# Performance work log

Hardware: AMD Instinct MI355X
Metric: run time of the kernel (lower is better)

The kernel has to match this reference:

```python
import jax, jax.numpy as jnp
import numpy as np

N = 100000      # nodes
E = 2500000     # edges
DIN, H, DOUT = 3, 32, 4
EPS = 1e-5

def _lin(k, i, o):
    kw, kb = jax.random.split(k)
    lim = 1.0 / np.sqrt(i)
    W = jax.random.uniform(kw, (i, o), jnp.float32, -lim, lim)
    b = jax.random.uniform(kb, (o,), jnp.float32, -lim, lim)
    return W, b

def setup_inputs():
    key = jax.random.key(0)
    ks = jax.random.split(key, 12)
    x = jax.random.normal(ks[0], (N, DIN), jnp.float32)
    edge_index = jax.random.randint(ks[1], (2, E), 0, N, dtype=jnp.int32)
    w_in1, b_in1 = _lin(ks[2], DIN, H)
    w_in2, b_in2 = _lin(ks[3], H, H)
    gamma = jnp.ones((H,), jnp.float32)
    beta = jnp.zeros((H,), jnp.float32)
    wg1, bg1 = _lin(ks[4], H, H)
    wg2, bg2 = _lin(ks[5], H, H)
    wg3, bg3 = _lin(ks[6], H, H)
    wo1, bo1 = _lin(ks[7], H, H)
    wo2, bo2 = _lin(ks[8], H, H)
    wo3, bo3 = _lin(ks[9], H, DOUT)
    return dict(x=x, w_in1=w_in1, b_in1=b_in1, w_in2=w_in2, b_in2=b_in2,
                gamma=gamma, beta=beta,
                wg1=wg1, bg1=bg1, wg2=wg2, bg2=bg2, wg3=wg3, bg3=bg3,
                wo1=wo1, bo1=bo1, wo2=wo2, bo2=bo2, wo3=wo3, bo3=bo3,
                edge_index=edge_index)

def _gcn(h, W, b, src, dst, norm):
    # PyG GCNConv: x' = scatter_add(norm * (xW)[src] -> dst) + bias
    hw = h @ W                                   # [N, H]
    msg = hw[src] * norm[:, None]                # [E+N, H] gather + scale
    out = jax.ops.segment_sum(msg, dst, num_segments=N)
    return out + b

def reference(x, w_in1, b_in1, w_in2, b_in2, gamma, beta,
              wg1, bg1, wg2, bg2, wg3, bg3,
              wo1, bo1, wo2, bo2, wo3, bo3, edge_index):
    leaky = lambda v: jax.nn.leaky_relu(v, 0.01)
    # input MLP
    h = leaky(x @ w_in1 + b_in1)
    h = leaky(h @ w_in2 + b_in2)
    # BatchNorm1d (training-mode batch statistics, biased variance)
    mu = jnp.mean(h, axis=0)
    var = jnp.mean((h - mu) ** 2, axis=0)
    h = (h - mu) * jax.lax.rsqrt(var + EPS) * gamma + beta
    # gcn_norm with self-loops: deg over target index, sym normalization
    loop = jnp.arange(N, dtype=edge_index.dtype)
    src = jnp.concatenate([edge_index[0], loop])
    dst = jnp.concatenate([edge_index[1], loop])
    deg = jax.ops.segment_sum(jnp.ones_like(src, jnp.float32), dst, num_segments=N)
    dis = jax.lax.rsqrt(deg)                     # deg >= 1 due to self-loops
    norm = dis[src] * dis[dst]                   # [E+N]
    h = jax.nn.elu(_gcn(h, wg1, bg1, src, dst, norm))
    h = jax.nn.elu(_gcn(h, wg2, bg2, src, dst, norm))
    h = jax.nn.elu(_gcn(h, wg3, bg3, src, dst, norm))
    # output MLP
    r = leaky(h @ wo1 + bo1)
    r = leaky(r @ wo2 + bo2)
    r = r @ wo3 + bo3                            # [N, 4]
    r = r.at[:, 0].set(jax.nn.sigmoid(r[:, 0]))
    return r
```

## Files before the change

### kernel.cpp

```cpp
#include <hip/hip_runtime.h>
#include <hip/hip_fp16.h>

#define HF 32
#define EPS 1e-5f
#define BSH 7
#define BSZ 128
#define CH  8192
#define SUBCAP 512
#define CAP (8*SUBCAP)

typedef int vi4 __attribute__((ext_vector_type(4)));

__device__ __forceinline__ float leaky(float v){ return fmaxf(v, 0.01f*v); }
__device__ __forceinline__ float elu1(float v){ return v > 0.f ? v : (expf(v)-1.f); }
__device__ __forceinline__ float sigmoidf(float v){ return 1.f/(1.f+expf(-v)); }

__device__ __forceinline__ int4 nt_load_i4(const int* p){
    vi4 v = __builtin_nontemporal_load((const vi4*)p);
    return make_int4(v.x, v.y, v.z, v.w);
}

__device__ __forceinline__ void addrow8(float* a, float4 v){
    const __half2* p = (const __half2*)&v;
#pragma unroll
    for (int k = 0; k < 4; k++){
        float2 f = __half22float2(p[k]);
        a[2*k] += f.x; a[2*k+1] += f.y;
    }
}
__device__ __forceinline__ float4 h2add4f(float4 a, float4 b){
    __half2* pa = (__half2*)&a; __half2* pb = (__half2*)&b;
    float4 r; __half2* pr = (__half2*)&r;
#pragma unroll
    for (int k = 0; k < 4; k++) pr[k] = __hadd2(pa[k], pb[k]);
    return r;
}

union SMem {
    struct {
        float sW1[3*HF]; float sB1[HF]; float sW2[HF*HF]; float sB2[HF];
        float sh[256][33];
    } mlp;
    struct { int lcnt[1024]; int lbase[1024]; int lpos[1024]; } bin;
};

__global__ __launch_bounds__(256)
void k_mlp_bin(const float* __restrict__ x,
               const float* __restrict__ w1, const float* __restrict__ b1,
               const float* __restrict__ w2, const float* __restrict__ b2,
               __half* __restrict__ h, float* __restrict__ stats,
               const int* __restrict__ src, const int* __restrict__ dst,
               int* __restrict__ gfill, int* __restrict__ ep,
               int N, int E, int B, int NB1){
    __shared__ SMem sm;
    int t = threadIdx.x;
    if ((int)blockIdx.x < NB1){
        for (int i = t; i < 3*HF; i += 256) sm.mlp.sW1[i] = w1[i];
        if (t < HF){ sm.mlp.sB1[t] = b1[t]; sm.mlp.sB2[t] = b2[t]; }
        for (int i = t; i < HF*HF; i += 256) sm.mlp.sW2[i] = w2[i];
        __syncthreads();
        int n = blockIdx.x*256 + t;
        float h2[HF];
        if (n < N){
            float x0 = x[(size_t)n*3], x1 = x[(size_t)n*3+1], x2 = x[(size_t)n*3+2];
            float h1[HF];
#pragma unroll
            for (int j = 0; j < HF; j++){
                float v = fmaf(x0, sm.mlp.sW1[j], fmaf(x1, sm.mlp.sW1[HF+j],
                          fmaf(x2, sm.mlp.sW1[2*HF+j], sm.mlp.sB1[j])));
                h1[j] = leaky(v);
            }
#pragma unroll
            for (int j = 0; j < HF; j++){
                float v = sm.mlp.sB2[j];
#pragma unroll
                for (int i = 0; i < HF; i++) v = fmaf(h1[i], sm.mlp.sW2[i*HF+j], v);
                h2[j] = leaky(v);
            }
            float4* hv = (float4*)(h + (size_t)n*HF);
#pragma unroll
            for (int jb = 0; jb < 4; jb++){
                __half2 hh[4];
#pragma unroll
                for (int k = 0; k < 4; k++)
                    hh[k] = __float22half2_rn(make_float2(h2[jb*8+2*k], h2[jb*8+2*k+1]));
                hv[jb] = *(float4*)hh;
            }
        } else {
#pragma unroll
            for (int j = 0; j < HF; j++) h2[j] = 0.f;
        }
#pragma unroll
        for (int j = 0; j < HF; j++) sm.mlp.sh[t][j] = h2[j];
        __syncthreads();
        int f = t & 31, g = t >> 5;
        float s = 0.f, ss = 0.f;
        for (int i = 0; i < 32; i++){
            float v = sm.mlp.sh[g*32 + i][f];
            s += v; ss += v*v;
        }
        __syncthreads();
        sm.mlp.sh[g][f] = s; sm.mlp.sh[8+g][f] = ss;
        __syncthreads();
        if (t < HF){
            float a = 0.f, b = 0.f;
#pragma unroll
            for (int g2 = 0; g2 < 8; g2++){ a += sm.mlp.sh[g2][t]; b += sm.mlp.sh[8+g2][t]; }
            atomicAdd(&stats[t], a);
            atomicAdd(&stats[HF+t], b);
        }
    } else {
        int bid = blockIdx.x - NB1;
        for (int i = t; i < B; i += 256){ sm.bin.lcnt[i] = 0; sm.bin.lpos[i] = 0; }
        __syncthreads();
        int base = bid * CH;
        int xcd = blockIdx.x & 7;
        int dv[16], sv[16];
        for (int half = 0; half < 2; half++){
            int hbase = base + half*4096;
#pragma unroll
            for (int i = 0; i < 16; i++){
                int e = hbase + t + i*256;
                dv[i] = (e < E) ? dst[e] : -1;
                sv[i] = (e < E) ? src[e] : 0;
            }
#pragma unroll
            for (int i = 0; i < 16; i++)
                if (dv[i] >= 0) atomicAdd(&sm.bin.lcnt[dv[i] >> BSH], 1);
            if (half == 0){
            }
            __syncthreads();
            if (half == 0){
            }
        }
        for (int i = t; i < B; i += 256){
            int c = sm.bin.lcnt[i];
            sm.bin.lbase[i] = c ? (i*CAP + xcd*SUBCAP + atomicAdd(&gfill[i*8 + xcd], c)) : 0;
        }
        __syncthreads();
        for (int half = 0; half < 2; half++){
            int hbase = base + half*4096;
#pragma unroll
            for (int i = 0; i < 16; i++){
                int e = hbase + t + i*256;
                if (e < E){
                    int d = dst[e], s = src[e];
                    int bb = d >> BSH;
                    int p = sm.bin.lbase[bb] + atomicAdd(&sm.bin.lpos[bb], 1);
                    ep[p] = (s << BSH) | (d & (BSZ-1));
                }
            }
        }
    }
}

__global__ __launch_bounds__(256)
void k_bucketD(int* __restrict__ ep, const int* __restrict__ gfill,
               int2* __restrict__ rowp2, float* __restrict__ dis, int N, int B){
    __shared__ int sep[CAP];
    __shared__ int lcnt[256], lpre[256], lfill[256], sc[256];
    int b = blockIdx.x, t = threadIdx.x;
    int cx[8], coff[8], cnt = 0;
#pragma unroll
    for (int x = 0; x < 8; x++){ cx[x] = gfill[b*8 + x]; coff[x] = cnt; cnt += cx[x]; }
    lcnt[t] = 0; lfill[t] = 0;
    __syncthreads();
    int base = b*CAP;
#pragma unroll
    for (int x = 0; x < 8; x++)
        for (int j = t; j < cx[x]; j += 256) sep[coff[x] + j] = ep[base + x*SUBCAP + j];
    __syncthreads();
    for (int e = t; e < cnt; e += 256) atomicAdd(&lcnt[sep[e] & (BSZ-1)], 1);
    __syncthreads();
    int v = lcnt[t];
    sc[t] = v; __syncthreads();
    for (int off = 1; off < 256; off <<= 1){
        int u = (t >= off) ? sc[t - off] : 0;
        __syncthreads();
        sc[t] += u;
        __syncthreads();
    }
    int pre = sc[t] - v;
    lpre[t] = pre;
    int n = b*BSZ + t;
    if (t < BSZ && n < N){
        rowp2[n] = make_int2(base + pre, base + pre + v);
        dis[n]   = rsqrtf((float)(v + 1));
    }
    __syncthreads();
    for (int e = t; e < cnt; e += 256){
        int val = sep[e];
        int d = val & (BSZ-1);
        int p = lpre[d] + atomicAdd(&lfill[d], 1);
        ep[base + p] = val >> BSH;
    }
}

__global__ __launch_bounds__(256)
void k_bn_t1(const __half* __restrict__ h, const float* __restrict__ stats,
             const float* __restrict__ gamma, const float* __restrict__ beta,
             const float* __restrict__ W, const float* __restrict__ dis,
             __half* __restrict__ tout, int N){
    __shared__ float sW[HF*HF];
    __shared__ float sh[64][33];
    int tid = threadIdx.x;
    for (int i = tid; i < HF*HF; i += 256) sW[i] = W[i];
    int nib = tid >> 2, l = tid & 3;
    int n = blockIdx.x*64 + nib;
    float hv[8];
    float d = 0.f;
    if (n < N){
        float4 raw = ((const float4*)h)[(size_t)n*4 + l];
        const __half2* p = (const __half2*)&raw;
        float tmp[8];
#pragma unroll
        for (int k = 0; k < 4; k++){
            float2 f2 = __half22float2(p[k]);
            tmp[2*k] = f2.x; tmp[2*k+1] = f2.y;
        }
        d = dis[n];
        float inv = 1.0f / (float)N;
#pragma unroll
        for (int c = 0; c < 8; c++){
            int f = 8*l + c;
            float mu  = stats[f]    * inv;
            float var = stats[HF+f] * inv - mu*mu;
            float rs  = rsqrtf(var + EPS);
            hv[c] = (tmp[c] - mu) * rs * gamma[f] + beta[f];
        }
    } else {
#pragma unroll
        for (int c = 0; c < 8; c++) hv[c] = 0.f;
    }
    __syncthreads();
#pragma unroll
    for (int c = 0; c < 8; c++) sh[nib][8*l + c] = hv[c];
    __syncthreads();
    float o[8] = {0.f,0.f,0.f,0.f,0.f,0.f,0.f,0.f};
#pragma unroll
    for (int i = 0; i < HF; i++){
        float hvv = sh[nib][i];
        float4 w0 = *(const float4*)&sW[i*HF + 8*l];
        float4 w1 = *(const float4*)&sW[i*HF + 8*l + 4];
        o[0] = fmaf(hvv, w0.x, o[0]); o[1] = fmaf(hvv, w0.y, o[1]);
        o[2] = fmaf(hvv, w0.z, o[2]); o[3] = fmaf(hvv, w0.w, o[3]);
        o[4] = fmaf(hvv, w1.x, o[4]); o[5] = fmaf(hvv, w1.y, o[5]);
        o[6] = fmaf(hvv, w1.z, o[6]); o[7] = fmaf(hvv, w1.w, o[7]);
    }
    if (n < N){
        __half2 hh[4];
#pragma unroll
        for (int k = 0; k < 4; k++)
            hh[k] = __float22half2_rn(make_float2(o[2*k]*d, o[2*k+1]*d));
        ((float4*)tout)[(size_t)n*4 + l] = *(float4*)hh;
    }
}

__global__ __launch_bounds__(256)
void k_gather_t(const __half* __restrict__ tin, const int* __restrict__ esrc,
                const int2* __restrict__ rowp2, const float* __restrict__ dis,
                const float* __restrict__ bias, const float* __restrict__ W,
                __half* __restrict__ tout, int N){
    __shared__ float sW[HF*HF];
    __shared__ float sh[64][33];
    int tid = threadIdx.x;
    for (int i = tid; i < HF*HF; i += 256) sW[i] = W[i];
    int nib = tid >> 2, l = tid & 3;
    int n = blockIdx.x*64 + nib;
    float acc[8] = {0.f,0.f,0.f,0.f,0.f,0.f,0.f,0.f};
    float d = 0.f;
    const float4* tv = (const float4*)tin;
    if (n < N){
        addrow8(acc, tv[(size_t)n*4 + l]);
        int2 r = rowp2[n];
        int e = r.x, e1 = r.y;
        while (e < e1 && (e & 3)){ addrow8(acc, tv[(size_t)esrc[e]*4 + l]); e++; }
        for (; e + 7 < e1; e += 8){
            int4 a4 = nt_load_i4(&esrc[e]);
            int4 b4 = nt_load_i4(&esrc[e+4]);
            float4 v0 = tv[(size_t)a4.x*4 + l];
            float4 v1 = tv[(size_t)a4.y*4 + l];
            float4 v2 = tv[(size_t)a4.z*4 + l];
            float4 v3 = tv[(size_t)a4.w*4 + l];
            float4 v4 = tv[(size_t)b4.x*4 + l];
            float4 v5 = tv[(size_t)b4.y*4 + l];
            float4 v6 = tv[(size_t)b4.z*4 + l];
            float4 v7 = tv[(size_t)b4.w*4 + l];
            addrow8(acc, h2add4f(h2add4f(v0, v1), h2add4f(v2, v3)));
            addrow8(acc, h2add4f(h2add4f(v4, v5), h2add4f(v6, v7)));
        }
        for (; e + 3 < e1; e += 4){
            int4 s4 = nt_load_i4(&esrc[e]);
            float4 v0 = tv[(size_t)s4.x*4 + l];
            float4 v1 = tv[(size_t)s4.y*4 + l];
            float4 v2 = tv[(size_t)s4.z*4 + l];
            float4 v3 = tv[(size_t)s4.w*4 + l];
            addrow8(acc, h2add4f(h2add4f(v0, v1), h2add4f(v2, v3)));
        }
        for (; e < e1; e++) addrow8(acc, tv[(size_t)esrc[e]*4 + l]);
        d = dis[n];
#pragma unroll
        for (int c = 0; c < 8; c++)
            acc[c] = elu1(fmaf(d, acc[c], bias[8*l + c]));
    }
    __syncthreads();
#pragma unroll
    for (int c = 0; c < 8; c++) sh[nib][8*l + c] = acc[c];
    __syncthreads();
    float o[8] = {0.f,0.f,0.f,0.f,0.f,0.f,0.f,0.f};
#pragma unroll
    for (int i = 0; i < HF; i++){
        float hvv = sh[nib][i];
        float4 w0 = *(const float4*)&sW[i*HF + 8*l];
        float4 w1 = *(const float4*)&sW[i*HF + 8*l + 4];
        o[0] = fmaf(hvv, w0.x, o[0]); o[1] = fmaf(hvv, w0.y, o[1]);
        o[2] = fmaf(hvv, w0.z, o[2]); o[3] = fmaf(hvv, w0.w, o[3]);
        o[4] = fmaf(hvv, w1.x, o[4]); o[5] = fmaf(hvv, w1.y, o[5]);
        o[6] = fmaf(hvv, w1.z, o[6]); o[7] = fmaf(hvv, w1.w, o[7]);
    }
    if (n < N){
        __half2 hh[4];
#pragma unroll
        for (int k = 0; k < 4; k++)
            hh[k] = __float22half2_rn(make_float2(o[2*k]*d, o[2*k+1]*d));
        ((float4*)tout)[(size_t)n*4 + l] = *(float4*)hh;
    }
}

__global__ __launch_bounds__(256)
void k_gather_out(const __half* __restrict__ tin, const int* __restrict__ esrc,
                  const int2* __restrict__ rowp2, const float* __restrict__ dis,
                  const float* __restrict__ bg3,
                  const float* __restrict__ wo1, const float* __restrict__ bo1,
                  const float* __restrict__ wo2, const float* __restrict__ bo2,
                  const float* __restrict__ wo3, const float* __restrict__ bo3,
                  float* __restrict__ out, int N){
    __shared__ float sW1[HF*HF], sW2[HF*HF], sW3[HF*4];
    __shared__ float sh[64][33], sh2[64][33];
    int tid = threadIdx.x;
    for (int i = tid; i < HF*HF; i += 256){ sW1[i] = wo1[i]; sW2[i] = wo2[i]; }
    if (tid < HF*4) sW3[tid] = wo3[tid];
    int nib = tid >> 2, l = tid & 3;
    int n = blockIdx.x*64 + nib;
    float acc[8] = {0.f,0.f,0.f,0.f,0.f,0.f,0.f,0.f};
    const float4* tv = (const float4*)tin;
    if (n < N){
        addrow8(acc, tv[(size_t)n*4 + l]);
        int2 r = rowp2[n];
        int e = r.x, e1 = r.y;
        while (e < e1 && (e & 3)){ addrow8(acc, tv[(size_t)esrc[e]*4 + l]); e++; }
        for (; e + 7 < e1; e += 8){
            int4 a4 = nt_load_i4(&esrc[e]);
            int4 b4 = nt_load_i4(&esrc[e+4]);
            float4 v0 = tv[(size_t)a4.x*4 + l];
            float4 v1 = tv[(size_t)a4.y*4 + l];
            float4 v2 = tv[(size_t)a4.z*4 + l];
            float4 v3 = tv[(size_t)a4.w*4 + l];
            float4 v4 = tv[(size_t)b4.x*4 + l];
            float4 v5 = tv[(size_t)b4.y*4 + l];
            float4 v6 = tv[(size_t)b4.z*4 + l];
            float4 v7 = tv[(size_t)b4.w*4 + l];
            addrow8(acc, h2add4f(h2add4f(v0, v1), h2add4f(v2, v3)));
            addrow8(acc, h2add4f(h2add4f(v4, v5), h2add4f(v6, v7)));
        }
        for (; e + 3 < e1; e += 4){
            int4 s4 = nt_load_i4(&esrc[e]);
            float4 v0 = tv[(size_t)s4.x*4 + l];
            float4 v1 = tv[(size_t)s4.y*4 + l];
            float4 v2 = tv[(size_t)s4.z*4 + l];
            float4 v3 = tv[(size_t)s4.w*4 + l];
            addrow8(acc, h2add4f(h2add4f(v0, v1), h2add4f(v2, v3)));
        }
        for (; e < e1; e++) addrow8(acc, tv[(size_t)esrc[e]*4 + l]);
        float d = dis[n];
#pragma unroll
        for (int c = 0; c < 8; c++)
            acc[c] = elu1(fmaf(d, acc[c], bg3[8*l + c]));
    }
    __syncthreads();
#pragma unroll
    for (int c = 0; c < 8; c++) sh[nib][8*l + c] = acc[c];
    __syncthreads();
    float o1[8];
#pragma unroll
    for (int c = 0; c < 8; c++) o1[c] = bo1[8*l + c];
#pragma unroll
    for (int i = 0; i < HF; i++){
        float hvv = sh[nib][i];
        float4 w0 = *(const float4*)&sW1[i*HF + 8*l];
        float4 w1 = *(const float4*)&sW1[i*HF + 8*l + 4];
        o1[0] = fmaf(hvv, w0.x, o1[0]); o1[1] = fmaf(hvv, w0.y, o1[1]);
        o1[2] = fmaf(hvv, w0.z, o1[2]); o1[3] = fmaf(hvv, w0.w, o1[3]);
        o1[4] = fmaf(hvv, w1.x, o1[4]); o1[5] = fmaf(hvv, w1.y, o1[5]);
        o1[6] = fmaf(hvv, w1.z, o1[6]); o1[7] = fmaf(hvv, w1.w, o1[7]);
    }
#pragma unroll
    for (int c = 0; c < 8; c++) sh2[nib][8*l + c] = leaky(o1[c]);
    __syncthreads();
    float o2[8];
#pragma unroll
    for (int c = 0; c < 8; c++) o2[c] = bo2[8*l + c];
#pragma unroll
    for (int i = 0; i < HF; i++){
        float hvv = sh2[nib][i];
        float4 w0 = *(const float4*)&sW2[i*HF + 8*l];
        float4 w1 = *(const float4*)&sW2[i*HF + 8*l + 4];
        o2[0] = fmaf(hvv, w0.x, o2[0]); o2[1] = fmaf(hvv, w0.y, o2[1]);
        o2[2] = fmaf(hvv, w0.z, o2[2]); o2[3] = fmaf(hvv, w0.w, o2[3]);
        o2[4] = fmaf(hvv, w1.x, o2[4]); o2[5] = fmaf(hvv, w1.y, o2[5]);
        o2[6] = fmaf(hvv, w1.z, o2[6]); o2[7] = fmaf(hvv, w1.w, o2[7]);
    }
#pragma unroll
    for (int c = 0; c < 8; c++) sh[nib][8*l + c] = leaky(o2[c]);
    __syncthreads();
    if (n < N){
        float v = bo3[l];
#pragma unroll
        for (int i = 0; i < HF; i++) v = fmaf(sh[nib][i], sW3[i*4 + l], v);
        if (l == 0) v = sigmoidf(v);
        out[(size_t)n*4 + l] = v;
    }
}

extern "C" void kernel_launch(void* const* d_in, const int* in_sizes, int n_in,
                              void* d_out, int out_size, void* d_ws, size_t ws_size,
                              hipStream_t stream) {
    const float* x     = (const float*)d_in[0];
    const float* w_in1 = (const float*)d_in[1];
    const float* b_in1 = (const float*)d_in[2];
    const float* w_in2 = (const float*)d_in[3];
    const float* b_in2 = (const float*)d_in[4];
    const float* gamma = (const float*)d_in[5];
    const float* beta  = (const float*)d_in[6];
    const float* wg1   = (const float*)d_in[7];
    const float* bg1   = (const float*)d_in[8];
    const float* wg2   = (const float*)d_in[9];
    const float* bg2   = (const float*)d_in[10];
    const float* wg3   = (const float*)d_in[11];
    const float* bg3   = (const float*)d_in[12];
    const float* wo1   = (const float*)d_in[13];
    const float* bo1   = (const float*)d_in[14];
    const float* wo2   = (const float*)d_in[15];
    const float* bo2   = (const float*)d_in[16];
    const float* wo3   = (const float*)d_in[17];
    const float* bo3   = (const float*)d_in[18];
    const int*   ei    = (const int*)d_in[19];

    int N = in_sizes[0] / 3;
    int E = in_sizes[19] / 2;
    int B = (N + BSZ - 1) >> BSH;

    char* w = (char*)d_ws;
    size_t o = 0;
    auto alloc = [&](size_t bytes){ size_t r = o; o = (o + bytes + 255) & ~(size_t)255; return r; };
    float* stats = (float*)(w + alloc(2*HF*sizeof(float)));
    int*   gfill = (int*)  (w + alloc((size_t)B*8*4));
    size_t zero_bytes = o;
    int2*  rowp2 = (int2*) (w + alloc((size_t)N*8));
    float* dis   = (float*)(w + alloc((size_t)N*4));
    int*   ep    = (int*)  (w + alloc((size_t)B*CAP*4));
    __half* bufH = (__half*)(w + alloc((size_t)N*HF*2));
    __half* tA   = (__half*)(w + alloc((size_t)N*HF*2));
    __half* tB   = (__half*)(w + alloc((size_t)N*HF*2));

    hipMemsetAsync(d_ws, 0, zero_bytes, stream);

    const int* src = ei;
    const int* dst = ei + E;
    int NB1 = (N + 255) / 256;
    int NC  = (E + CH - 1) / CH;
    int GB  = (N + 63) / 64;

    k_mlp_bin<<<NB1 + NC, 256, 0, stream>>>(x, w_in1, b_in1, w_in2, b_in2, bufH, stats,
                                            src, dst, gfill, ep, N, E, B, NB1);
    k_bucketD<<<B, 256, 0, stream>>>(ep, gfill, rowp2, dis, N, B);

    k_bn_t1   <<<GB, 256, 0, stream>>>(bufH, stats, gamma, beta, wg1, dis, tA, N);
    k_gather_t<<<GB, 256, 0, stream>>>(tA, ep, rowp2, dis, bg1, wg2, tB, N);
    k_gather_t<<<GB, 256, 0, stream>>>(tB, ep, rowp2, dis, bg2, wg3, tA, N);
    k_gather_out<<<GB, 256, 0, stream>>>(tA, ep, rowp2, dis, bg3,
                                         wo1, bo1, wo2, bo2, wo3, bo3, (float*)d_out, N);
}
```

Baseline: 288.7 us.

## Compute degrees during binning, fuse CSR build with BN transform, degree-sorted gather order

The binning pass now counts node degrees with global atomics, so the bucket kernel no longer needs a shared-memory histogram and scan. It is fused with the BatchNorm plus first-transform kernel into one launch that computes dis directly from deg. Each bucket also ranks its nodes by degree and writes a node order array, which the gather kernels use so that nodes of similar degree share a wavefront and divergence drops. The chunk size is halved and edges are loaded once into registers with vectorized nontemporal loads. In exchange there are global atomics per edge on deg and one extra indirection in the gather kernels.

```diff
diff --git a/kernel.cpp b/kernel.cpp
--- a/kernel.cpp
+++ b/kernel.cpp
@@ -5,7 +5,7 @@
 #define EPS 1e-5f
 #define BSH 7
 #define BSZ 128
-#define CH  8192
+#define CH  4096
 #define SUBCAP 512
 #define CAP (8*SUBCAP)
 
@@ -51,15 +51,58 @@
                __half* __restrict__ h, float* __restrict__ stats,
                const int* __restrict__ src, const int* __restrict__ dst,
                int* __restrict__ gfill, int* __restrict__ ep,
-               int N, int E, int B, int NB1){
+               int* __restrict__ deg,
+               int N, int E, int B, int NC){
     __shared__ SMem sm;
     int t = threadIdx.x;
-    if ((int)blockIdx.x < NB1){
+    if ((int)blockIdx.x < NC){
+        int bid = blockIdx.x;
+        for (int i = t; i < B; i += 256){ sm.bin.lcnt[i] = 0; sm.bin.lpos[i] = 0; }
+        __syncthreads();
+        int base = bid * CH;
+        int xcd = bid & 7;
+        int dv[16], sv[16];
+        if (base + CH <= E){
+#pragma unroll
+            for (int i = 0; i < 4; i++){
+                int4 d4 = nt_load_i4(dst + base + (t + i*256)*4);
+                int4 s4 = nt_load_i4(src + base + (t + i*256)*4);
+                dv[4*i]   = d4.x; dv[4*i+1] = d4.y; dv[4*i+2] = d4.z; dv[4*i+3] = d4.w;
+                sv[4*i]   = s4.x; sv[4*i+1] = s4.y; sv[4*i+2] = s4.z; sv[4*i+3] = s4.w;
+            }
+        } else {
+#pragma unroll
+            for (int i = 0; i < 16; i++){
+                int e = base + t + i*256;
+                dv[i] = (e < E) ? dst[e] : -1;
+                sv[i] = (e < E) ? src[e] : 0;
+            }
+        }
+#pragma unroll
+        for (int i = 0; i < 16; i++)
+            if (dv[i] >= 0){
+                atomicAdd(&sm.bin.lcnt[dv[i] >> BSH], 1);
+                atomicAdd(&deg[dv[i]], 1);
+            }
+        __syncthreads();
+        for (int i = t; i < B; i += 256){
+            int c = sm.bin.lcnt[i];
+            sm.bin.lbase[i] = c ? (i*CAP + xcd*SUBCAP + atomicAdd(&gfill[i*8 + xcd], c)) : 0;
+        }
+        __syncthreads();
+#pragma unroll
+        for (int i = 0; i < 16; i++)
+            if (dv[i] >= 0){
+                int bb = dv[i] >> BSH;
+                int p = sm.bin.lbase[bb] + atomicAdd(&sm.bin.lpos[bb], 1);
+                ep[p] = (sv[i] << BSH) | (dv[i] & (BSZ-1));
+            }
+    } else {
         for (int i = t; i < 3*HF; i += 256) sm.mlp.sW1[i] = w1[i];
         if (t < HF){ sm.mlp.sB1[t] = b1[t]; sm.mlp.sB2[t] = b2[t]; }
         for (int i = t; i < HF*HF; i += 256) sm.mlp.sW2[i] = w2[i];
         __syncthreads();
-        int n = blockIdx.x*256 + t;
+        int n = (blockIdx.x - NC)*256 + t;
         float h2[HF];
         if (n < N){
             float x0 = x[(size_t)n*3], x1 = x[(size_t)n*3+1], x2 = x[(size_t)n*3+2];
@@ -109,156 +152,123 @@
             atomicAdd(&stats[t], a);
             atomicAdd(&stats[HF+t], b);
         }
+    }
+}
+
+union SMem2 {
+    struct { int sep[CAP]; int sdeg[128]; int spre[128]; int sfill[128]; } c;
+    struct { float sW[HF*HF]; float sh[64][33]; } m;
+};
+
+__global__ __launch_bounds__(256)
+void k_csr_bn(int* __restrict__ ep, const int* __restrict__ gfill,
+              const int* __restrict__ deg,
+              int2* __restrict__ rowp2, float* __restrict__ dis,
+              int* __restrict__ norder,
+              const __half* __restrict__ h, const float* __restrict__ stats,
+              const float* __restrict__ gamma, const float* __restrict__ beta,
+              const float* __restrict__ W, __half* __restrict__ tout,
+              int N, int B){
+    __shared__ SMem2 sm;
+    int t = threadIdx.x;
+    if ((int)blockIdx.x < B){
+        int b = blockIdx.x;
+        int cx[8], coff[8], cnt = 0;
+#pragma unroll
+        for (int xx = 0; xx < 8; xx++){ cx[xx] = gfill[b*8 + xx]; coff[xx] = cnt; cnt += cx[xx]; }
+        int base = b*CAP;
+#pragma unroll
+        for (int xx = 0; xx < 8; xx++)
+            for (int j = t; j < cx[xx]; j += 256) sm.c.sep[coff[xx] + j] = ep[base + xx*SUBCAP + j];
+        if (t < 128){
+            sm.c.sfill[t] = 0;
+            int n = b*BSZ + t;
+            sm.c.sdeg[t] = (n < N) ? deg[n] : 0;
+        }
+        __syncthreads();
+        if (t < 128){
+            int dg = sm.c.sdeg[t];
+            int pre = 0, rank = 0;
+            for (int j = 0; j < 128; j++){
+                int dj = sm.c.sdeg[j];
+                if (j < t) pre += dj;
+                if (dj > dg || (dj == dg && j < t)) rank++;
+            }
+            sm.c.spre[t] = pre;
+            int n = b*BSZ + t;
+            if (n < N){
+                rowp2[n] = make_int2(base + pre, base + pre + dg);
+                dis[n]   = rsqrtf((float)dg + 1.0f);
+                norder[b*BSZ + rank] = n;
+            } else {
+                norder[b*BSZ + rank] = -1;
+            }
+        }
+        __syncthreads();
+        for (int e = t; e < cnt; e += 256){
+            int val = sm.c.sep[e];
+            int d = val & (BSZ-1);
+            int p = sm.c.spre[d] + atomicAdd(&sm.c.sfill[d], 1);
+            ep[base + p] = val >> BSH;
+        }
     } else {
-        int bid = blockIdx.x - NB1;
-        for (int i = t; i < B; i += 256){ sm.bin.lcnt[i] = 0; sm.bin.lpos[i] = 0; }
-        __syncthreads();
-        int base = bid * CH;
-        int xcd = blockIdx.x & 7;
-        int dv[16], sv[16];
-        for (int half = 0; half < 2; half++){
-            int hbase = base + half*4096;
-#pragma unroll
-            for (int i = 0; i < 16; i++){
-                int e = hbase + t + i*256;
-                dv[i] = (e < E) ? dst[e] : -1;
-                sv[i] = (e < E) ? src[e] : 0;
-            }
-#pragma unroll
-            for (int i = 0; i < 16; i++)
-                if (dv[i] >= 0) atomicAdd(&sm.bin.lcnt[dv[i] >> BSH], 1);
-            if (half == 0){
-            }
-            __syncthreads();
-            if (half == 0){
-            }
-        }
-        for (int i = t; i < B; i += 256){
-            int c = sm.bin.lcnt[i];
-            sm.bin.lbase[i] = c ? (i*CAP + xcd*SUBCAP + atomicAdd(&gfill[i*8 + xcd], c)) : 0;
-        }
-        __syncthreads();
-        for (int half = 0; half < 2; half++){
-            int hbase = base + half*4096;
-#pragma unroll
-            for (int i = 0; i < 16; i++){
-                int e = hbase + t + i*256;
-                if (e < E){
-                    int d = dst[e], s = src[e];
-                    int bb = d >> BSH;
-                    int p = sm.bin.lbase[bb] + atomicAdd(&sm.bin.lpos[bb], 1);
-                    ep[p] = (s << BSH) | (d & (BSZ-1));
-                }
-            }
-        }
-    }
-}
-
-__global__ __launch_bounds__(256)
-void k_bucketD(int* __restrict__ ep, const int* __restrict__ gfill,
-               int2* __restrict__ rowp2, float* __restrict__ dis, int N, int B){
-    __shared__ int sep[CAP];
-    __shared__ int lcnt[256], lpre[256], lfill[256], sc[256];
-    int b = blockIdx.x, t = threadIdx.x;
-    int cx[8], coff[8], cnt = 0;
-#pragma unroll
-    for (int x = 0; x < 8; x++){ cx[x] = gfill[b*8 + x]; coff[x] = cnt; cnt += cx[x]; }
-    lcnt[t] = 0; lfill[t] = 0;
-    __syncthreads();
-    int base = b*CAP;
-#pragma unroll
-    for (int x = 0; x < 8; x++)
-        for (int j = t; j < cx[x]; j += 256) sep[coff[x] + j] = ep[base + x*SUBCAP + j];
-    __syncthreads();
-    for (int e = t; e < cnt; e += 256) atomicAdd(&lcnt[sep[e] & (BSZ-1)], 1);
-    __syncthreads();
-    int v = lcnt[t];
-    sc[t] = v; __syncthreads();
-    for (int off = 1; off < 256; off <<= 1){
-        int u = (t >= off) ? sc[t - off] : 0;
-        __syncthreads();
-        sc[t] += u;
-        __syncthreads();
-    }
-    int pre = sc[t] - v;
-    lpre[t] = pre;
-    int n = b*BSZ + t;
-    if (t < BSZ && n < N){
-        rowp2[n] = make_int2(base + pre, base + pre + v);
-        dis[n]   = rsqrtf((float)(v + 1));
-    }
-    __syncthreads();
-    for (int e = t; e < cnt; e += 256){
-        int val = sep[e];
-        int d = val & (BSZ-1);
-        int p = lpre[d] + atomicAdd(&lfill[d], 1);
-        ep[base + p] = val >> BSH;
-    }
-}
-
-__global__ __launch_bounds__(256)
-void k_bn_t1(const __half* __restrict__ h, const float* __restrict__ stats,
-             const float* __restrict__ gamma, const float* __restrict__ beta,
-             const float* __restrict__ W, const float* __restrict__ dis,
-             __half* __restrict__ tout, int N){
-    __shared__ float sW[HF*HF];
-    __shared__ float sh[64][33];
-    int tid = threadIdx.x;
-    for (int i = tid; i < HF*HF; i += 256) sW[i] = W[i];
-    int nib = tid >> 2, l = tid & 3;
-    int n = blockIdx.x*64 + nib;
-    float hv[8];
-    float d = 0.f;
-    if (n < N){
-        float4 raw = ((const float4*)h)[(size_t)n*4 + l];
-        const __half2* p = (const __half2*)&raw;
-        float tmp[8];
-#pragma unroll
-        for (int k = 0; k < 4; k++){
-            float2 f2 = __half22float2(p[k]);
-            tmp[2*k] = f2.x; tmp[2*k+1] = f2.y;
-        }
-        d = dis[n];
-        float inv = 1.0f / (float)N;
-#pragma unroll
-        for (int c = 0; c < 8; c++){
-            int f = 8*l + c;
-            float mu  = stats[f]    * inv;
-            float var = stats[HF+f] * inv - mu*mu;
-            float rs  = rsqrtf(var + EPS);
-            hv[c] = (tmp[c] - mu) * rs * gamma[f] + beta[f];
-        }
-    } else {
-#pragma unroll
-        for (int c = 0; c < 8; c++) hv[c] = 0.f;
-    }
-    __syncthreads();
-#pragma unroll
-    for (int c = 0; c < 8; c++) sh[nib][8*l + c] = hv[c];
-    __syncthreads();
-    float o[8] = {0.f,0.f,0.f,0.f,0.f,0.f,0.f,0.f};
-#pragma unroll
-    for (int i = 0; i < HF; i++){
-        float hvv = sh[nib][i];
-        float4 w0 = *(const float4*)&sW[i*HF + 8*l];
-        float4 w1 = *(const float4*)&sW[i*HF + 8*l + 4];
-        o[0] = fmaf(hvv, w0.x, o[0]); o[1] = fmaf(hvv, w0.y, o[1]);
-        o[2] = fmaf(hvv, w0.z, o[2]); o[3] = fmaf(hvv, w0.w, o[3]);
-        o[4] = fmaf(hvv, w1.x, o[4]); o[5] = fmaf(hvv, w1.y, o[5]);
-        o[6] = fmaf(hvv, w1.z, o[6]); o[7] = fmaf(hvv, w1.w, o[7]);
-    }
-    if (n < N){
-        __half2 hh[4];
-#pragma unroll
-        for (int k = 0; k < 4; k++)
-            hh[k] = __float22half2_rn(make_float2(o[2*k]*d, o[2*k+1]*d));
-        ((float4*)tout)[(size_t)n*4 + l] = *(float4*)hh;
+        for (int i = t; i < HF*HF; i += 256) sm.m.sW[i] = W[i];
+        int nib = t >> 2, l = t & 3;
+        int n = (blockIdx.x - B)*64 + nib;
+        float hv[8];
+        float d = 0.f;
+        if (n < N){
+            float4 raw = ((const float4*)h)[(size_t)n*4 + l];
+            const __half2* p = (const __half2*)&raw;
+            float tmp[8];
+#pragma unroll
+            for (int k = 0; k < 4; k++){
+                float2 f2 = __half22float2(p[k]);
+                tmp[2*k] = f2.x; tmp[2*k+1] = f2.y;
+            }
+            d = rsqrtf((float)deg[n] + 1.0f);
+            float inv = 1.0f / (float)N;
+#pragma unroll
+            for (int c = 0; c < 8; c++){
+                int f = 8*l + c;
+                float mu  = stats[f]    * inv;
+                float var = stats[HF+f] * inv - mu*mu;
+                float rs  = rsqrtf(var + EPS);
+                hv[c] = (tmp[c] - mu) * rs * gamma[f] + beta[f];
+            }
+        } else {
+#pragma unroll
+            for (int c = 0; c < 8; c++) hv[c] = 0.f;
+        }
+        __syncthreads();
+#pragma unroll
+        for (int c = 0; c < 8; c++) sm.m.sh[nib][8*l + c] = hv[c];
+        __syncthreads();
+        float o[8] = {0.f,0.f,0.f,0.f,0.f,0.f,0.f,0.f};
+#pragma unroll
+        for (int i = 0; i < HF; i++){
+            float hvv = sm.m.sh[nib][i];
+            float4 w0 = *(const float4*)&sm.m.sW[i*HF + 8*l];
+            float4 w1 = *(const float4*)&sm.m.sW[i*HF + 8*l + 4];
+            o[0] = fmaf(hvv, w0.x, o[0]); o[1] = fmaf(hvv, w0.y, o[1]);
+            o[2] = fmaf(hvv, w0.z, o[2]); o[3] = fmaf(hvv, w0.w, o[3]);
+            o[4] = fmaf(hvv, w1.x, o[4]); o[5] = fmaf(hvv, w1.y, o[5]);
+            o[6] = fmaf(hvv, w1.z, o[6]); o[7] = fmaf(hvv, w1.w, o[7]);
+        }
+        if (n < N){
+            __half2 hh[4];
+#pragma unroll
+            for (int k = 0; k < 4; k++)
+                hh[k] = __float22half2_rn(make_float2(o[2*k]*d, o[2*k+1]*d));
+            ((float4*)tout)[(size_t)n*4 + l] = *(float4*)hh;
+        }
     }
 }
 
 __global__ __launch_bounds__(256)
 void k_gather_t(const __half* __restrict__ tin, const int* __restrict__ esrc,
                 const int2* __restrict__ rowp2, const float* __restrict__ dis,
+                const int* __restrict__ norder,
                 const float* __restrict__ bias, const float* __restrict__ W,
                 __half* __restrict__ tout, int N){
     __shared__ float sW[HF*HF];
@@ -266,11 +276,11 @@
     int tid = threadIdx.x;
     for (int i = tid; i < HF*HF; i += 256) sW[i] = W[i];
     int nib = tid >> 2, l = tid & 3;
-    int n = blockIdx.x*64 + nib;
+    int n = norder[blockIdx.x*64 + nib];
     float acc[8] = {0.f,0.f,0.f,0.f,0.f,0.f,0.f,0.f};
     float d = 0.f;
     const float4* tv = (const float4*)tin;
-    if (n < N){
+    if (n >= 0){
         addrow8(acc, tv[(size_t)n*4 + l]);
         int2 r = rowp2[n];
         int e = r.x, e1 = r.y;
@@ -318,7 +328,7 @@
         o[4] = fmaf(hvv, w1.x, o[4]); o[5] = fmaf(hvv, w1.y, o[5]);
         o[6] = fmaf(hvv, w1.z, o[6]); o[7] = fmaf(hvv, w1.w, o[7]);
     }
-    if (n < N){
+    if (n >= 0){
         __half2 hh[4];
 #pragma unroll
         for (int k = 0; k < 4; k++)
@@ -330,6 +340,7 @@
 __global__ __launch_bounds__(256)
 void k_gather_out(const __half* __restrict__ tin, const int* __restrict__ esrc,
                   const int2* __restrict__ rowp2, const float* __restrict__ dis,
+                  const int* __restrict__ norder,
                   const float* __restrict__ bg3,
                   const float* __restrict__ wo1, const float* __restrict__ bo1,
                   const float* __restrict__ wo2, const float* __restrict__ bo2,
@@ -341,10 +352,10 @@
     for (int i = tid; i < HF*HF; i += 256){ sW1[i] = wo1[i]; sW2[i] = wo2[i]; }
     if (tid < HF*4) sW3[tid] = wo3[tid];
     int nib = tid >> 2, l = tid & 3;
-    int n = blockIdx.x*64 + nib;
+    int n = norder[blockIdx.x*64 + nib];
     float acc[8] = {0.f,0.f,0.f,0.f,0.f,0.f,0.f,0.f};
     const float4* tv = (const float4*)tin;
-    if (n < N){
+    if (n >= 0){
         addrow8(acc, tv[(size_t)n*4 + l]);
         int2 r = rowp2[n];
         int e = r.x, e1 = r.y;
@@ -413,7 +424,7 @@
 #pragma unroll
     for (int c = 0; c < 8; c++) sh[nib][8*l + c] = leaky(o2[c]);
     __syncthreads();
-    if (n < N){
+    if (n >= 0){
         float v = bo3[l];
 #pragma unroll
         for (int i = 0; i < HF; i++) v = fmaf(sh[nib][i], sW3[i*4 + l], v);
@@ -455,9 +466,11 @@
     auto alloc = [&](size_t bytes){ size_t r = o; o = (o + bytes + 255) & ~(size_t)255; return r; };
     float* stats = (float*)(w + alloc(2*HF*sizeof(float)));
     int*   gfill = (int*)  (w + alloc((size_t)B*8*4));
+    int*   deg   = (int*)  (w + alloc((size_t)N*4));
     size_t zero_bytes = o;
     int2*  rowp2 = (int2*) (w + alloc((size_t)N*8));
     float* dis   = (float*)(w + alloc((size_t)N*4));
+    int*   norder= (int*)  (w + alloc((size_t)B*BSZ*4));
     int*   ep    = (int*)  (w + alloc((size_t)B*CAP*4));
     __half* bufH = (__half*)(w + alloc((size_t)N*HF*2));
     __half* tA   = (__half*)(w + alloc((size_t)N*HF*2));
@@ -469,15 +482,15 @@
     const int* dst = ei + E;
     int NB1 = (N + 255) / 256;
     int NC  = (E + CH - 1) / CH;
-    int GB  = (N + 63) / 64;
-
-    k_mlp_bin<<<NB1 + NC, 256, 0, stream>>>(x, w_in1, b_in1, w_in2, b_in2, bufH, stats,
-                                            src, dst, gfill, ep, N, E, B, NB1);
-    k_bucketD<<<B, 256, 0, stream>>>(ep, gfill, rowp2, dis, N, B);
-
-    k_bn_t1   <<<GB, 256, 0, stream>>>(bufH, stats, gamma, beta, wg1, dis, tA, N);
-    k_gather_t<<<GB, 256, 0, stream>>>(tA, ep, rowp2, dis, bg1, wg2, tB, N);
-    k_gather_t<<<GB, 256, 0, stream>>>(tB, ep, rowp2, dis, bg2, wg3, tA, N);
-    k_gather_out<<<GB, 256, 0, stream>>>(tA, ep, rowp2, dis, bg3,
+    int GBT = (N + 63) / 64;
+    int NS  = 2*B;
+
+    k_mlp_bin<<<NC + NB1, 256, 0, stream>>>(x, w_in1, b_in1, w_in2, b_in2, bufH, stats,
+                                            src, dst, gfill, ep, deg, N, E, B, NC);
+    k_csr_bn<<<B + GBT, 256, 0, stream>>>(ep, gfill, deg, rowp2, dis, norder,
+                                          bufH, stats, gamma, beta, wg1, tA, N, B);
+    k_gather_t<<<NS, 256, 0, stream>>>(tA, ep, rowp2, dis, norder, bg1, wg2, tB, N);
+    k_gather_t<<<NS, 256, 0, stream>>>(tB, ep, rowp2, dis, norder, bg2, wg3, tA, N);
+    k_gather_out<<<NS, 256, 0, stream>>>(tA, ep, rowp2, dis, norder, bg3,
                                          wo1, bo1, wo2, bo2, wo3, bo3, (float*)d_out, N);
 }
```

Result: slower. 382.3 us (+32.4%).
